# Kernel optimization log

Hardware: AMD Instinct MI355X
Metric: run time of the kernel (lower is better)

Reference implementation:

```python
import jax, jax.numpy as jnp
import numpy as np

N = 50000; E = 1600000; F = 128; H = 128; C = 40; G = 4
GRID = jnp.linspace(-2.0, 2.0, G)          # FastKAN default grid [-2, 2]
DENOM = 4.0 / (G - 1)                      # (grid_max - grid_min) / (num_grids - 1)
EPS = 1e-5
DIMS = [(F, H), (H, H), (F + 2 * H, C)]    # conv0, conv1, conv_out (skip concat)


def setup_inputs() -> dict:
    key = jax.random.key(0)
    ks = iter(jax.random.split(key, 64))
    inp = {}
    inp["x"] = jax.random.normal(next(ks), (N, F), jnp.float32)
    inp["edge_index"] = jax.random.randint(next(ks), (2, E), 0, N)
    for i, (di, do) in enumerate(DIMS):
        inp[f"c{i}_ln_g"] = jnp.ones((di,), jnp.float32)
        inp[f"c{i}_ln_b"] = jnp.zeros((di,), jnp.float32)
        inp[f"c{i}_sw"] = jax.random.normal(next(ks), (do, di * G), jnp.float32) * 0.1
        inp[f"c{i}_sb"] = jnp.zeros((do,), jnp.float32)
        inp[f"c{i}_bw"] = jax.random.normal(next(ks), (do, di), jnp.float32) * (1.0 / np.sqrt(di))
        inp[f"c{i}_bb"] = jnp.zeros((do,), jnp.float32)
        inp[f"c{i}_bias"] = jnp.zeros((do,), jnp.float32)   # GCNConv output bias
    inp["bn_g"] = jnp.ones((H,), jnp.float32)
    inp["bn_b"] = jnp.zeros((H,), jnp.float32)
    return inp


def _fkan(h, lg, lb, sw, sb, bw, bb):
    # FastKANLayer: LayerNorm -> RBF basis -> spline linear, plus SiLU base branch
    mu = h.mean(-1, keepdims=True)
    var = jnp.mean(jnp.square(h - mu), -1, keepdims=True)
    hn = (h - mu) * jax.lax.rsqrt(var + EPS) * lg + lb
    basis = jnp.exp(-jnp.square((hn[..., None] - GRID) / DENOM))  # [N, d, G]
    basis = basis.reshape(h.shape[0], -1)                          # [N, d*G]
    return basis @ sw.T + sb + jax.nn.silu(h) @ bw.T + bb


def _forward(x, edge_index, params, bn_g, bn_b):
    # gcn_norm with self-loops, symmetric normalization
    row = jnp.concatenate([edge_index[0], jnp.arange(N)])
    col = jnp.concatenate([edge_index[1], jnp.arange(N)])
    deg = jax.ops.segment_sum(jnp.ones_like(row, jnp.float32), col, num_segments=N)
    dis = jnp.where(deg > 0, jax.lax.rsqrt(jnp.maximum(deg, 1e-12)), 0.0)
    norm = dis[row] * dis[col]

    def conv(h, p):
        hw = _fkan(h, *p[:6])  # lin = FKANLayer applied before propagate
        return jax.ops.segment_sum(norm[:, None] * hw[row], col, num_segments=N) + p[6]

    def bn(h):  # BatchNorm1d, training-mode batch stats (biased var); dropout p=0
        mu = h.mean(0)
        var = jnp.mean(jnp.square(h - mu), 0)
        return (h - mu) * jax.lax.rsqrt(var + EPS) * bn_g + bn_b

    skips = [x]
    h = x
    for p in params[:-1]:
        h = bn(conv(h, p))
        skips.append(h)
    h = jnp.concatenate(skips, axis=1)  # skip=True
    return conv(h, params[-1])


def reference(x, edge_index, c0_ln_g, c0_ln_b, c0_sw, c0_sb, c0_bw, c0_bb, c0_bias,
              c1_ln_g, c1_ln_b, c1_sw, c1_sb, c1_bw, c1_bb, c1_bias,
              c2_ln_g, c2_ln_b, c2_sw, c2_sb, c2_bw, c2_bb, c2_bias, bn_g, bn_b):
    params = [
        (c0_ln_g, c0_ln_b, c0_sw, c0_sb, c0_bw, c0_bb, c0_bias),
        (c1_ln_g, c1_ln_b, c1_sw, c1_sb, c1_bw, c1_bb, c1_bias),
        (c2_ln_g, c2_ln_b, c2_sw, c2_sb, c2_bw, c2_bb, c2_bias),
    ]
    return _forward(x, edge_index, params, bn_g, bn_b)
```

## Files before the change

### kernel.cpp

```cpp
#include <hip/hip_runtime.h>
#include <math.h>

constexpr int NN = 50000;
constexpr int NE = 1600000;
constexpr float LN_EPS = 1e-5f;

constexpr int NBKT  = 8;
constexpr int SPAN  = NN / NBKT;
constexpr int CHUNK = 8192;
constexpr int NB1   = (NE + CHUNK - 1) / CHUNK;
constexpr int NSB   = (NN + 255) / 256;

typedef __attribute__((ext_vector_type(8))) short short8;
typedef __attribute__((ext_vector_type(4))) float f32x4;

__device__ __forceinline__ short f2bf(float f)
{
    unsigned u = __builtin_bit_cast(unsigned, f);
    u += 0x7fffu + ((u >> 16) & 1u);
    return (short)(u >> 16);
}

__device__ __forceinline__ float2 bf2x2(unsigned p)
{
    float2 r;
    r.x = __builtin_bit_cast(float, p << 16);
    r.y = __builtin_bit_cast(float, p & 0xffff0000u);
    return r;
}

__global__ __launch_bounds__(256) void csr_hist(const int* __restrict__ col,
                                                int* __restrict__ degi,
                                                int* __restrict__ histo)
{
    __shared__ int hcnt[NBKT];
    const int tid = threadIdx.x;
    if (tid < NBKT) hcnt[tid] = 0;
    __syncthreads();
    const int e0 = blockIdx.x * CHUNK;
    const int e1 = min(e0 + CHUNK, NE);
    for (int e = e0 + tid; e < e1; e += 256) {
        int c = col[e];
        atomicAdd(&degi[c], 1);
        atomicAdd(&hcnt[(unsigned)c / (unsigned)SPAN], 1);
    }
    __syncthreads();
    if (tid < NBKT) histo[tid * NB1 + blockIdx.x] = hcnt[tid];
}

__global__ __launch_bounds__(256) void csr_scan2(int* __restrict__ histo)
{
    constexpr int M = NBKT * NB1;
    constexpr int T = (M + 255) / 256;
    __shared__ int part[256];
    const int t = threadIdx.x;
    int v[T];
    int s = 0;
    #pragma unroll
    for (int j = 0; j < T; ++j) {
        int i = t * T + j;
        v[j] = (i < M) ? histo[i] : 0;
        s += v[j];
    }
    part[t] = s;
    __syncthreads();
    for (int d = 1; d < 256; d <<= 1) {
        int add = (t >= d) ? part[t - d] : 0;
        __syncthreads();
        part[t] += add;
        __syncthreads();
    }
    int run = part[t] - s;
    #pragma unroll
    for (int j = 0; j < T; ++j) {
        int i = t * T + j;
        if (i < M) { histo[i] = run; run += v[j]; }
    }
}

__global__ __launch_bounds__(256) void csr_part(const int* __restrict__ ei,
                                                const int* __restrict__ histo,
                                                uint2* __restrict__ staging)
{
    __shared__ int lcur[NBKT];
    const int tid = threadIdx.x;
    if (tid < NBKT) lcur[tid] = histo[tid * NB1 + blockIdx.x];
    __syncthreads();
    const int e0 = blockIdx.x * CHUNK;
    const int e1 = min(e0 + CHUNK, NE);
    for (int e = e0 + tid; e < e1; e += 256) {
        int r = ei[e];
        int c = ei[NE + e];
        int slot = atomicAdd(&lcur[(unsigned)c / (unsigned)SPAN], 1);
        staging[slot] = make_uint2((unsigned)r, (unsigned)c);
    }
}

template<int PB2>
__global__ __launch_bounds__(256) void csr_scatter(const uint2* __restrict__ staging,
                                                   const int* __restrict__ off,
                                                   int* __restrict__ cur,
                                                   int* __restrict__ rows)
{
    const int b   = blockIdx.x & (NBKT - 1);
    const int blk = blockIdx.x >> 3;
    const int base = off[b * SPAN];
    const int end  = off[(b + 1) * SPAN];
    for (int i = base + blk * 256 + threadIdx.x; i < end; i += PB2 * 256) {
        uint2 e = staging[i];
        int p = off[e.y] + atomicAdd(&cur[e.y], 1);
        rows[p] = (int)e.x;
    }
}

__global__ void dis_kernel(const int* __restrict__ degi, float* __restrict__ dis)
{
    int i = blockIdx.x * 256 + threadIdx.x;
    if (i < NN) dis[i] = rsqrtf((float)degi[i] + 1.0f);
}

__global__ __launch_bounds__(256) void scan_p1(const int* __restrict__ deg,
                                               int* __restrict__ off,
                                               int* __restrict__ partials)
{
    __shared__ int sh[256];
    const int t = threadIdx.x;
    const int i = blockIdx.x * 256 + t;
    int v = (i < NN) ? deg[i] : 0;
    sh[t] = v;
    __syncthreads();
    for (int d = 1; d < 256; d <<= 1) {
        int add = (t >= d) ? sh[t - d] : 0;
        __syncthreads();
        sh[t] += add;
        __syncthreads();
    }
    if (i < NN) off[i] = sh[t] - v;
    if (t == 255) partials[blockIdx.x] = sh[255];
}

__global__ __launch_bounds__(256) void scan_p2(int* __restrict__ partials)
{
    __shared__ int sh[256];
    const int t = threadIdx.x;
    int v = (t < NSB) ? partials[t] : 0;
    sh[t] = v;
    __syncthreads();
    for (int d = 1; d < 256; d <<= 1) {
        int add = (t >= d) ? sh[t - d] : 0;
        __syncthreads();
        sh[t] += add;
        __syncthreads();
    }
    if (t < NSB) partials[t] = sh[t] - v;
    if (t == 255) partials[NSB] = sh[255];
}

__global__ __launch_bounds__(256) void scan_p3(int* __restrict__ off,
                                               const int* __restrict__ partials)
{
    const int i = blockIdx.x * 256 + threadIdx.x;
    if (i < NN) off[i] += partials[blockIdx.x];
    if (i == 0) off[NN] = partials[NSB];
}

__global__ void pack_frag(const float* __restrict__ sw, const float* __restrict__ bw,
                          short* __restrict__ wtf, int D, int OT, int DO, int total)
{
    int idx = blockIdx.x * 256 + threadIdx.x;
    if (idx >= total) return;
    int j8   = idx & 7;
    int lane = (idx >> 3) & 63;
    int rest = idx >> 9;
    int ot = rest % OT, kk = rest / OT;
    int g4 = lane >> 4;
    int s  = kk * 8 + j8;
    int f  = g4 * (D / 4) + s / 5;
    int g5 = s % 5;
    int o  = ot * 16 + (lane & 15);
    float val = 0.f;
    if (o < DO) val = (g5 < 4) ? sw[o * D * 4 + f * 4 + g5] : bw[o * D + f];
    wtf[idx] = f2bf(val);
}

__global__ void bn_id(float2* __restrict__ bnp)
{
    bnp[threadIdx.x] = make_float2(1.0f, 0.0f);
}

__global__ void bn_final(const float* __restrict__ stats, const float* __restrict__ g,
                         const float* __restrict__ b, float2* __restrict__ dst)
{
    int c = threadIdx.x;
    float mu  = stats[c] * (1.0f / NN);
    float var = stats[c + 128] * (1.0f / NN) - mu * mu;
    float rs  = rsqrtf(var + LN_EPS);
    float sc  = rs * g[c];
    dst[c] = make_float2(sc, b[c] - mu * sc);
}

template<int DO, int OT, int KKC, bool BN>
__global__ __launch_bounds__(256, 4) void fkan_rd(
    const float* __restrict__ s0, const float2* __restrict__ bnp,
    const float* __restrict__ ln_g, const float* __restrict__ ln_b,
    const short* __restrict__ wtf, const float* __restrict__ sb, const float* __restrict__ bb,
    short* __restrict__ out)
{
    const int tid  = threadIdx.x;
    const int wv   = tid >> 6, lane = tid & 63;
    const int m    = lane & 15, q = lane >> 4;
    const int gnode = blockIdx.x * 64 + wv * 16 + m;
    const int snode = (gnode < NN) ? gnode : (NN - 1);

    float4 v[8];
    float sum = 0.f, sq = 0.f;
    #pragma unroll
    for (int i = 0; i < 8; ++i) {
        int f = q * 32 + i * 4;
        float4 t = *(const float4*)&s0[snode * 128 + f];
        if constexpr (BN) {
            float4 ba = *(const float4*)&bnp[f];
            float4 bc = *(const float4*)&bnp[f + 2];
            t.x = fmaf(t.x, ba.x, ba.y);
            t.y = fmaf(t.y, ba.z, ba.w);
            t.z = fmaf(t.z, bc.x, bc.y);
            t.w = fmaf(t.w, bc.z, bc.w);
        }
        v[i] = t;
        sum += (t.x + t.y) + (t.z + t.w);
        sq  += (t.x * t.x + t.y * t.y) + (t.z * t.z + t.w * t.w);
    }
    sum += __shfl_xor(sum, 16); sum += __shfl_xor(sum, 32);
    sq  += __shfl_xor(sq, 16);  sq  += __shfl_xor(sq, 32);
    const float mu   = sum * (1.0f / 128.0f);
    const float rstd = rsqrtf(sq * (1.0f / 128.0f) - mu * mu + LN_EPS);

    f32x4 acc[OT];
    #pragma unroll
    for (int ot = 0; ot < OT; ++ot) acc[ot] = f32x4{0.f, 0.f, 0.f, 0.f};

    union AU { unsigned u[4]; short8 s; };

    #pragma unroll
    for (int pl = 0; pl < KKC / 5; ++pl) {
        float hn[8], slv[8];
        {
            float4 lg0 = *(const float4*)&ln_g[q * 32 + pl * 8];
            float4 lg1 = *(const float4*)&ln_g[q * 32 + pl * 8 + 4];
            float4 lb0 = *(const float4*)&ln_b[q * 32 + pl * 8];
            float4 lb1 = *(const float4*)&ln_b[q * 32 + pl * 8 + 4];
            float4 va = v[pl * 2], vb = v[pl * 2 + 1];
            hn[0] = (va.x - mu) * rstd * lg0.x + lb0.x;
            hn[1] = (va.y - mu) * rstd * lg0.y + lb0.y;
            hn[2] = (va.z - mu) * rstd * lg0.z + lb0.z;
            hn[3] = (va.w - mu) * rstd * lg0.w + lb0.w;
            hn[4] = (vb.x - mu) * rstd * lg1.x + lb1.x;
            hn[5] = (vb.y - mu) * rstd * lg1.y + lb1.y;
            hn[6] = (vb.z - mu) * rstd * lg1.z + lb1.z;
            hn[7] = (vb.w - mu) * rstd * lg1.w + lb1.w;
            slv[0] = va.x / (1.0f + __expf(-va.x));
            slv[1] = va.y / (1.0f + __expf(-va.y));
            slv[2] = va.z / (1.0f + __expf(-va.z));
            slv[3] = va.w / (1.0f + __expf(-va.w));
            slv[4] = vb.x / (1.0f + __expf(-vb.x));
            slv[5] = vb.y / (1.0f + __expf(-vb.y));
            slv[6] = vb.z / (1.0f + __expf(-vb.z));
            slv[7] = vb.w / (1.0f + __expf(-vb.w));
        }
        const short* bp = wtf + (pl * 5) * OT * 512 + lane * 8;
        #pragma unroll
        for (int c = 0; c < 5; ++c) {
            AU a;
            #pragma unroll
            for (int i = 0; i < 4; ++i) {
                unsigned v2[2];
                #pragma unroll
                for (int h = 0; h < 2; ++h) {
                    int s  = c * 8 + 2 * i + h;
                    int fl = s / 5;
                    int g  = s % 5;
                    if (g == 4) {
                        v2[h] = (unsigned)(unsigned short)f2bf(slv[fl]);
                    } else {
                        float t = hn[fl] * 0.75f + (1.5f - (float)g);
                        float e = __expf(-t * t);
                        v2[h] = (unsigned)(unsigned short)f2bf(e);
                    }
                }
                a.u[i] = (v2[0] & 0xffffu) | (v2[1] << 16);
            }
            #pragma unroll
            for (int ot = 0; ot < OT; ++ot) {
                short8 b = *(const short8*)(bp + (c * OT + ot) * 512);
                acc[ot] = __builtin_amdgcn_mfma_f32_16x16x32_bf16(a.s, b, acc[ot], 0, 0, 0);
            }
        }
    }

    const int nrow0 = blockIdx.x * 64 + wv * 16 + q * 4;
    #pragma unroll
    for (int ot = 0; ot < OT; ++ot) {
        int o = ot * 16 + m;
        if (o < DO) {
            float cb = sb[o] + bb[o];
            #pragma unroll
            for (int r = 0; r < 4; ++r) {
                int nr = nrow0 + r;
                if (nr < NN) out[nr * DO + o] = f2bf(acc[ot][r] + cb);
            }
        }
    }
}

template<int D, int DO, int OT, int KKC, int NODES, int WPE, bool RAWLDS, bool BN>
__global__ __launch_bounds__(NODES * 4, WPE) void fkan_reg(
    const float* __restrict__ s0, const float* __restrict__ s1, const float* __restrict__ s2,
    const float2* __restrict__ bnp,
    const float* __restrict__ ln_g, const float* __restrict__ ln_b,
    const short* __restrict__ wtf, const float* __restrict__ sb, const float* __restrict__ bb,
    short* __restrict__ out)
{
    constexpr int BW   = D / 4;
    constexpr int GBS  = BW + 1;
    constexpr int RS   = 4 * GBS + 1;
    constexpr int PPC  = KKC / 5;
    constexpr int NV   = RAWLDS ? 1 : (BW / 4);
    __shared__ unsigned pkL[NODES * RS];

    const int tid = threadIdx.x;
    const int anode = tid >> 2, q = tid & 3;
    const int gnode = blockIdx.x * NODES + anode;
    const int snode = (gnode < NN) ? gnode : (NN - 1);
    unsigned* prow = &pkL[anode * RS + q * GBS];

    float mu, rstd;
    float4 va[NV];
    {
        float sum = 0.f, sq = 0.f;
        #pragma unroll
        for (int i4 = 0; i4 < BW / 4; ++i4) {
            int f = q * BW + i4 * 4;
            const float* src = (D == 128) ? s0 : ((f < 128) ? s0 : (f < 256) ? s1 : s2);
            float4 v = *(const float4*)&src[snode * 128 + (f & 127)];
            if constexpr (BN) {
                float4 ba = *(const float4*)&bnp[f];
                float4 bc = *(const float4*)&bnp[f + 2];
                v.x = fmaf(v.x, ba.x, ba.y);
                v.y = fmaf(v.y, ba.z, ba.w);
                v.z = fmaf(v.z, bc.x, bc.y);
                v.w = fmaf(v.w, bc.z, bc.w);
            }
            if constexpr (RAWLDS) {
                prow[i4 * 4 + 0] = __builtin_bit_cast(unsigned, v.x);
                prow[i4 * 4 + 1] = __builtin_bit_cast(unsigned, v.y);
                prow[i4 * 4 + 2] = __builtin_bit_cast(unsigned, v.z);
                prow[i4 * 4 + 3] = __builtin_bit_cast(unsigned, v.w);
            } else {
                va[i4] = v;
            }
            sum += (v.x + v.y) + (v.z + v.w);
            sq  += (v.x * v.x + v.y * v.y) + (v.z * v.z + v.w * v.w);
        }
        sum += __shfl_xor(sum, 1); sum += __shfl_xor(sum, 2);
        sq  += __shfl_xor(sq, 1);  sq  += __shfl_xor(sq, 2);
        mu   = sum * (1.0f / D);
        rstd = rsqrtf(sq * (1.0f / D) - mu * mu + LN_EPS);
    }

    #pragma unroll
    for (int i4 = 0; i4 < BW / 4; ++i4) {
        int f = q * BW + i4 * 4;
        float4 v;
        if constexpr (RAWLDS) {
            v.x = __builtin_bit_cast(float, prow[i4 * 4 + 0]);
            v.y = __builtin_bit_cast(float, prow[i4 * 4 + 1]);
            v.z = __builtin_bit_cast(float, prow[i4 * 4 + 2]);
            v.w = __builtin_bit_cast(float, prow[i4 * 4 + 3]);
        } else {
            v = va[i4];
        }
        float4 lg = *(const float4*)&ln_g[f];
        float4 lb = *(const float4*)&ln_b[f];
        float hn[4], sl[4];
        hn[0] = (v.x - mu) * rstd * lg.x + lb.x;
        hn[1] = (v.y - mu) * rstd * lg.y + lb.y;
        hn[2] = (v.z - mu) * rstd * lg.z + lb.z;
        hn[3] = (v.w - mu) * rstd * lg.w + lb.w;
        sl[0] = v.x / (1.0f + __expf(-v.x));
        sl[1] = v.y / (1.0f + __expf(-v.y));
        sl[2] = v.z / (1.0f + __expf(-v.z));
        sl[3] = v.w / (1.0f + __expf(-v.w));
        #pragma unroll
        for (int k = 0; k < 4; ++k)
            prow[i4 * 4 + k] = ((unsigned)(unsigned short)f2bf(hn[k]) << 16)
                             | ((unsigned)(unsigned short)f2bf(sl[k]) & 0xffffu);
    }
    __syncthreads();

    const int wv = tid >> 6, lane = tid & 63;
    const int m = lane & 15, g4 = lane >> 4;
    const unsigned* pkb = &pkL[(wv * 16 + m) * RS + g4 * GBS];

    f32x4 acc[OT];
    #pragma unroll
    for (int ot = 0; ot < OT; ++ot) acc[ot] = f32x4{0.f, 0.f, 0.f, 0.f};

    union AU { unsigned u[4]; short8 s; };

    for (int pl = 0; pl < PPC; ++pl) {
        const unsigned* pp = pkb + pl * 8;
        const short* bp = wtf + (pl * 5) * OT * 512 + lane * 8;
        #pragma unroll
        for (int c = 0; c < 5; ++c) {
            constexpr int FL0[5] = {0, 1, 3, 4, 6};
            constexpr int NF[5]  = {2, 3, 2, 3, 2};
            unsigned p[3];
            float h75[3];
            #pragma unroll
            for (int i = 0; i < 3; ++i) {
                if (i < NF[c]) {
                    p[i]   = pp[FL0[c] + i];
                    h75[i] = __builtin_bit_cast(float, p[i] & 0xffff0000u) * 0.75f;
                }
            }
            AU a;
            #pragma unroll
            for (int i = 0; i < 4; ++i) {
                unsigned v2[2];
                #pragma unroll
                for (int h = 0; h < 2; ++h) {
                    int sl = c * 8 + 2 * i + h;
                    int fl = sl / 5 - FL0[c];
                    int g  = sl % 5;
                    if (g == 4) {
                        v2[h] = p[fl] & 0xffffu;
                    } else {
                        float t = h75[fl] + (1.5f - (float)g);
                        float e = __expf(-t * t);
                        v2[h] = (unsigned)(unsigned short)f2bf(e);
                    }
                }
                a.u[i] = (v2[0] & 0xffffu) | (v2[1] << 16);
            }
            #pragma unroll
            for (int ot = 0; ot < OT; ++ot) {
                short8 b = *(const short8*)(bp + (c * OT + ot) * 512);
                acc[ot] = __builtin_amdgcn_mfma_f32_16x16x32_bf16(a.s, b, acc[ot], 0, 0, 0);
            }
        }
    }

    const int nrow0 = blockIdx.x * NODES + wv * 16 + g4 * 4;
    #pragma unroll
    for (int ot = 0; ot < OT; ++ot) {
        int o = ot * 16 + m;
        if (o < DO) {
            float cb = sb[o] + bb[o];
            #pragma unroll
            for (int r = 0; r < 4; ++r) {
                int nr = nrow0 + r;
                if (nr < NN) out[nr * DO + o] = f2bf(acc[ot][r] + cb);
            }
        }
    }
}

template<int DO>
__global__ __launch_bounds__(64) void agg_gather_bf16(
    const int* __restrict__ off, const int* __restrict__ rows,
    const float* __restrict__ dis, const short* __restrict__ hwb,
    const float* __restrict__ bias, float* __restrict__ out)
{
    constexpr int ACT = DO / 2;
    const int n   = blockIdx.x;
    const int tid = threadIdx.x;
    __shared__ int   srow[64];
    __shared__ float swgt[64];

    const int e0 = off[n], e1 = off[n + 1];
    const float dn = dis[n];
    float ax = 0.f, ay = 0.f;
    if (tid < ACT) {
        unsigned p = *(const unsigned*)&hwb[n * DO + 2 * tid];
        float2 v = bf2x2(p);
        ax = dn * dn * v.x + bias[2 * tid];
        ay = dn * dn * v.y + bias[2 * tid + 1];
    }

    for (int t0 = e0; t0 < e1; t0 += 64) {
        const int nt = min(64, e1 - t0);
        if (tid < nt) {
            int r = rows[t0 + tid];
            srow[tid] = r;
            swgt[tid] = dn * dis[r];
        }
        __syncthreads();
        if (tid < ACT) {
            #pragma unroll 4
            for (int j = 0; j < nt; ++j) {
                unsigned p = *(const unsigned*)&hwb[srow[j] * DO + 2 * tid];
                float2 v = bf2x2(p);
                float w = swgt[j];
                ax += w * v.x;
                ay += w * v.y;
            }
        }
        __syncthreads();
    }
    if (tid < ACT) {
        out[n * DO + 2 * tid]     = ax;
        out[n * DO + 2 * tid + 1] = ay;
    }
}

__global__ void bn_stats(const float* __restrict__ h, float* __restrict__ stats)
{
    __shared__ float s1[256], s2[256];
    int c = threadIdx.x & 127;
    int half = threadIdx.x >> 7;
    float sum = 0.f, sq = 0.f;
    for (int n = blockIdx.x * 2 + half; n < NN; n += 512) {
        float v = h[n * 128 + c];
        sum += v; sq += v * v;
    }
    s1[threadIdx.x] = sum; s2[threadIdx.x] = sq;
    __syncthreads();
    if (half == 0) {
        s1[c] += s1[c + 128]; s2[c] += s2[c + 128];
        atomicAdd(&stats[c],        s1[c]);
        atomicAdd(&stats[c + 128],  s2[c]);
    }
}

extern "C" void kernel_launch(void* const* d_in, const int* in_sizes, int n_in,
                              void* d_out, int out_size, void* d_ws, size_t ws_size,
                              hipStream_t stream)
{
    auto F = [&](int i) { return (const float*)d_in[i]; };
    const float* x  = F(0);
    const int*   ei = (const int*)d_in[1];
    const float* bn_g = F(23);
    const float* bn_b = F(24);

    short*  wtf0 = (short*)d_ws;
    short*  wtf1 = wtf0 + 81920;
    short*  wtf2 = wtf1 + 81920;
    short*  hwb  = wtf2 + 92160;
    float*  dis  = (float*)(hwb + 6400000);
    float2* bnp  = (float2*)(dis + 50000);
    float*  h1   = (float*)(bnp + 384);
    float*  h2   = h1 + 6400000;
    float*  stats = h2 + 6400000;
    int*    degi = (int*)(stats + 256);
    int*    off  = degi + 50000;
    int*    cur  = off + 50001;
    int*    rows = cur + 50000;
    int*    histo = rows + NE;
    int*    partials = histo + NBKT * NB1;
    uint2*  staging = (uint2*)h1;
    float*  outf = (float*)d_out;

    (void)hipMemsetAsync(degi, 0, 50000 * sizeof(int), stream);
    (void)hipMemsetAsync(cur,  0, 50000 * sizeof(int), stream);
    csr_hist<<<NB1, 256, 0, stream>>>(ei + NE, degi, histo);
    dis_kernel<<<(NN + 255) / 256, 256, 0, stream>>>(degi, dis);
    scan_p1<<<NSB, 256, 0, stream>>>(degi, off, partials);
    scan_p2<<<1, 256, 0, stream>>>(partials);
    scan_p3<<<NSB, 256, 0, stream>>>(off, partials);
    csr_scan2<<<1, 256, 0, stream>>>(histo);
    csr_part<<<NB1, 256, 0, stream>>>(ei, histo, staging);
    csr_scatter<128><<<128 * NBKT, 256, 0, stream>>>(staging, off, cur, rows);

    pack_frag<<<(81920 + 255) / 256, 256, 0, stream>>>(F(4),  F(6),  wtf0, 128, 8, 128, 81920);
    pack_frag<<<(81920 + 255) / 256, 256, 0, stream>>>(F(11), F(13), wtf1, 128, 8, 128, 81920);
    pack_frag<<<(92160 + 255) / 256, 256, 0, stream>>>(F(18), F(20), wtf2, 384, 3, 40,  92160);
    bn_id<<<1, 128, 0, stream>>>(bnp);

    const int gridN64 = (NN + 63) / 64;
    const int gridN16 = (NN + 15) / 16;

    fkan_rd<128, 8, 20, false><<<gridN64, 256, 0, stream>>>(x,
        nullptr, F(2), F(3), wtf0, F(5), F(7), hwb);
    agg_gather_bf16<128><<<NN, 64, 0, stream>>>(off, rows, dis, hwb, F(8), h1);
    (void)hipMemsetAsync(stats, 0, 256 * sizeof(float), stream);
    bn_stats<<<256, 256, 0, stream>>>(h1, stats);
    bn_final<<<1, 128, 0, stream>>>(stats, bn_g, bn_b, bnp + 128);

    fkan_rd<128, 8, 20, true><<<gridN64, 256, 0, stream>>>(h1,
        bnp + 128, F(9), F(10), wtf1, F(12), F(14), hwb);
    agg_gather_bf16<128><<<NN, 64, 0, stream>>>(off, rows, dis, hwb, F(15), h2);
    (void)hipMemsetAsync(stats, 0, 256 * sizeof(float), stream);
    bn_stats<<<256, 256, 0, stream>>>(h2, stats);
    bn_final<<<1, 128, 0, stream>>>(stats, bn_g, bn_b, bnp + 256);

    fkan_reg<384, 40, 3, 60, 16, 2, true, true><<<gridN16, 64, 0, stream>>>(x, h1, h2,
        bnp, F(16), F(17), wtf2, F(19), F(21), hwb);
    agg_gather_bf16<40><<<NN, 64, 0, stream>>>(off, rows, dis, hwb, F(22), outf);
}
```

Baseline: 540.1 us.

## Split final-layer LayerNorm stats into separate kernel and compute basis in registers

```diff
diff --git a/kernel.cpp b/kernel.cpp
--- a/kernel.cpp
+++ b/kernel.cpp
@@ -197,6 +197,40 @@
     float rs  = rsqrtf(var + LN_EPS);
     float sc  = rs * g[c];
     dst[c] = make_float2(sc, b[c] - mu * sc);
+}
+
+template<int D>
+__global__ __launch_bounds__(256) void ln_stats(
+    const float* __restrict__ s0, const float* __restrict__ s1, const float* __restrict__ s2,
+    const float2* __restrict__ bnp, float2* __restrict__ murstd)
+{
+    constexpr int BW = D / 4;
+    const int tid = threadIdx.x;
+    const int anode = tid >> 2, q = tid & 3;
+    const int gnode = blockIdx.x * 64 + anode;
+    const int snode = (gnode < NN) ? gnode : (NN - 1);
+    float sum = 0.f, sq = 0.f;
+    #pragma unroll
+    for (int i4 = 0; i4 < BW / 4; ++i4) {
+        int f = q * BW + i4 * 4;
+        const float* src = (f < 128) ? s0 : (f < 256) ? s1 : s2;
+        float4 v = *(const float4*)&src[snode * 128 + (f & 127)];
+        float4 ba = *(const float4*)&bnp[f];
+        float4 bc = *(const float4*)&bnp[f + 2];
+        v.x = fmaf(v.x, ba.x, ba.y);
+        v.y = fmaf(v.y, ba.z, ba.w);
+        v.z = fmaf(v.z, bc.x, bc.y);
+        v.w = fmaf(v.w, bc.z, bc.w);
+        sum += (v.x + v.y) + (v.z + v.w);
+        sq  += (v.x * v.x + v.y * v.y) + (v.z * v.z + v.w * v.w);
+    }
+    sum += __shfl_xor(sum, 1); sum += __shfl_xor(sum, 2);
+    sq  += __shfl_xor(sq, 1);  sq  += __shfl_xor(sq, 2);
+    if (q == 0 && gnode < NN) {
+        float mu   = sum * (1.0f / D);
+        float rstd = rsqrtf(sq * (1.0f / D) - mu * mu + LN_EPS);
+        murstd[gnode] = make_float2(mu, rstd);
+    }
 }
 
 template<int DO, int OT, int KKC, bool BN>
@@ -312,94 +346,21 @@
     }
 }
 
-template<int D, int DO, int OT, int KKC, int NODES, int WPE, bool RAWLDS, bool BN>
-__global__ __launch_bounds__(NODES * 4, WPE) void fkan_reg(
+template<int DO, int OT, int KKC>
+__global__ __launch_bounds__(256, 4) void fkan_rd2(
     const float* __restrict__ s0, const float* __restrict__ s1, const float* __restrict__ s2,
-    const float2* __restrict__ bnp,
+    const float2* __restrict__ bnp, const float2* __restrict__ murstd,
     const float* __restrict__ ln_g, const float* __restrict__ ln_b,
     const short* __restrict__ wtf, const float* __restrict__ sb, const float* __restrict__ bb,
     short* __restrict__ out)
 {
-    constexpr int BW   = D / 4;
-    constexpr int GBS  = BW + 1;
-    constexpr int RS   = 4 * GBS + 1;
-    constexpr int PPC  = KKC / 5;
-    constexpr int NV   = RAWLDS ? 1 : (BW / 4);
-    __shared__ unsigned pkL[NODES * RS];
-
-    const int tid = threadIdx.x;
-    const int anode = tid >> 2, q = tid & 3;
-    const int gnode = blockIdx.x * NODES + anode;
+    const int tid  = threadIdx.x;
+    const int wv   = tid >> 6, lane = tid & 63;
+    const int m    = lane & 15, q = lane >> 4;
+    const int gnode = blockIdx.x * 64 + wv * 16 + m;
     const int snode = (gnode < NN) ? gnode : (NN - 1);
-    unsigned* prow = &pkL[anode * RS + q * GBS];
-
-    float mu, rstd;
-    float4 va[NV];
-    {
-        float sum = 0.f, sq = 0.f;
-        #pragma unroll
-        for (int i4 = 0; i4 < BW / 4; ++i4) {
-            int f = q * BW + i4 * 4;
-            const float* src = (D == 128) ? s0 : ((f < 128) ? s0 : (f < 256) ? s1 : s2);
-            float4 v = *(const float4*)&src[snode * 128 + (f & 127)];
-            if constexpr (BN) {
-                float4 ba = *(const float4*)&bnp[f];
-                float4 bc = *(const float4*)&bnp[f + 2];
-                v.x = fmaf(v.x, ba.x, ba.y);
-                v.y = fmaf(v.y, ba.z, ba.w);
-                v.z = fmaf(v.z, bc.x, bc.y);
-                v.w = fmaf(v.w, bc.z, bc.w);
-            }
-            if constexpr (RAWLDS) {
-                prow[i4 * 4 + 0] = __builtin_bit_cast(unsigned, v.x);
-                prow[i4 * 4 + 1] = __builtin_bit_cast(unsigned, v.y);
-                prow[i4 * 4 + 2] = __builtin_bit_cast(unsigned, v.z);
-                prow[i4 * 4 + 3] = __builtin_bit_cast(unsigned, v.w);
-            } else {
-                va[i4] = v;
-            }
-            sum += (v.x + v.y) + (v.z + v.w);
-            sq  += (v.x * v.x + v.y * v.y) + (v.z * v.z + v.w * v.w);
-        }
-        sum += __shfl_xor(sum, 1); sum += __shfl_xor(sum, 2);
-        sq  += __shfl_xor(sq, 1);  sq  += __shfl_xor(sq, 2);
-        mu   = sum * (1.0f / D);
-        rstd = rsqrtf(sq * (1.0f / D) - mu * mu + LN_EPS);
-    }
-
-    #pragma unroll
-    for (int i4 = 0; i4 < BW / 4; ++i4) {
-        int f = q * BW + i4 * 4;
-        float4 v;
-        if constexpr (RAWLDS) {
-            v.x = __builtin_bit_cast(float, prow[i4 * 4 + 0]);
-            v.y = __builtin_bit_cast(float, prow[i4 * 4 + 1]);
-            v.z = __builtin_bit_cast(float, prow[i4 * 4 + 2]);
-            v.w = __builtin_bit_cast(float, prow[i4 * 4 + 3]);
-        } else {
-            v = va[i4];
-        }
-        float4 lg = *(const float4*)&ln_g[f];
-        float4 lb = *(const float4*)&ln_b[f];
-        float hn[4], sl[4];
-        hn[0] = (v.x - mu) * rstd * lg.x + lb.x;
-        hn[1] = (v.y - mu) * rstd * lg.y + lb.y;
-        hn[2] = (v.z - mu) * rstd * lg.z + lb.z;
-        hn[3] = (v.w - mu) * rstd * lg.w + lb.w;
-        sl[0] = v.x / (1.0f + __expf(-v.x));
-        sl[1] = v.y / (1.0f + __expf(-v.y));
-        sl[2] = v.z / (1.0f + __expf(-v.z));
-        sl[3] = v.w / (1.0f + __expf(-v.w));
-        #pragma unroll
-        for (int k = 0; k < 4; ++k)
-            prow[i4 * 4 + k] = ((unsigned)(unsigned short)f2bf(hn[k]) << 16)
-                             | ((unsigned)(unsigned short)f2bf(sl[k]) & 0xffffu);
-    }
-    __syncthreads();
-
-    const int wv = tid >> 6, lane = tid & 63;
-    const int m = lane & 15, g4 = lane >> 4;
-    const unsigned* pkb = &pkL[(wv * 16 + m) * RS + g4 * GBS];
+    const float2 ms = murstd[snode];
+    const float mu = ms.x, rstd = ms.y;
 
     f32x4 acc[OT];
     #pragma unroll
@@ -407,35 +368,68 @@
 
     union AU { unsigned u[4]; short8 s; };
 
-    for (int pl = 0; pl < PPC; ++pl) {
-        const unsigned* pp = pkb + pl * 8;
+    #pragma unroll
+    for (int pl = 0; pl < KKC / 5; ++pl) {
+        const int fa = q * 96 + pl * 8;
+        const int fb = fa + 4;
+        float4 va, vb;
+        {
+            const float* sa = (fa < 128) ? s0 : (fa < 256) ? s1 : s2;
+            const float* sc = (fb < 128) ? s0 : (fb < 256) ? s1 : s2;
+            va = *(const float4*)&sa[snode * 128 + (fa & 127)];
+            vb = *(const float4*)&sc[snode * 128 + (fb & 127)];
+            float4 b0 = *(const float4*)&bnp[fa];
+            float4 b1 = *(const float4*)&bnp[fa + 2];
+            float4 b2 = *(const float4*)&bnp[fb];
+            float4 b3 = *(const float4*)&bnp[fb + 2];
+            va.x = fmaf(va.x, b0.x, b0.y);
+            va.y = fmaf(va.y, b0.z, b0.w);
+            va.z = fmaf(va.z, b1.x, b1.y);
+            va.w = fmaf(va.w, b1.z, b1.w);
+            vb.x = fmaf(vb.x, b2.x, b2.y);
+            vb.y = fmaf(vb.y, b2.z, b2.w);
+            vb.z = fmaf(vb.z, b3.x, b3.y);
+            vb.w = fmaf(vb.w, b3.z, b3.w);
+        }
+        float hn[8], slv[8];
+        {
+            float4 lg0 = *(const float4*)&ln_g[fa];
+            float4 lg1 = *(const float4*)&ln_g[fb];
+            float4 lb0 = *(const float4*)&ln_b[fa];
+            float4 lb1 = *(const float4*)&ln_b[fb];
+            hn[0] = (va.x - mu) * rstd * lg0.x + lb0.x;
+            hn[1] = (va.y - mu) * rstd * lg0.y + lb0.y;
+            hn[2] = (va.z - mu) * rstd * lg0.z + lb0.z;
+            hn[3] = (va.w - mu) * rstd * lg0.w + lb0.w;
+            hn[4] = (vb.x - mu) * rstd * lg1.x + lb1.x;
+            hn[5] = (vb.y - mu) * rstd * lg1.y + lb1.y;
+            hn[6] = (vb.z - mu) * rstd * lg1.z + lb1.z;
+            hn[7] = (vb.w - mu) * rstd * lg1.w + lb1.w;
+            slv[0] = va.x / (1.0f + __expf(-va.x));
+            slv[1] = va.y / (1.0f + __expf(-va.y));
+            slv[2] = va.z / (1.0f + __expf(-va.z));
+            slv[3] = va.w / (1.0f + __expf(-va.w));
+            slv[4] = vb.x / (1.0f + __expf(-vb.x));
+            slv[5] = vb.y / (1.0f + __expf(-vb.y));
+            slv[6] = vb.z / (1.0f + __expf(-vb.z));
+            slv[7] = vb.w / (1.0f + __expf(-vb.w));
+        }
         const short* bp = wtf + (pl * 5) * OT * 512 + lane * 8;
         #pragma unroll
         for (int c = 0; c < 5; ++c) {
-            constexpr int FL0[5] = {0, 1, 3, 4, 6};
-            constexpr int NF[5]  = {2, 3, 2, 3, 2};
-            unsigned p[3];
-            float h75[3];
-            #pragma unroll
-            for (int i = 0; i < 3; ++i) {
-                if (i < NF[c]) {
-                    p[i]   = pp[FL0[c] + i];
-                    h75[i] = __builtin_bit_cast(float, p[i] & 0xffff0000u) * 0.75f;
-                }
-            }
             AU a;
             #pragma unroll
             for (int i = 0; i < 4; ++i) {
                 unsigned v2[2];
                 #pragma unroll
                 for (int h = 0; h < 2; ++h) {
-                    int sl = c * 8 + 2 * i + h;
-                    int fl = sl / 5 - FL0[c];
-                    int g  = sl % 5;
+                    int s  = c * 8 + 2 * i + h;
+                    int fl = s / 5;
+                    int g  = s % 5;
                     if (g == 4) {
-                        v2[h] = p[fl] & 0xffffu;
+                        v2[h] = (unsigned)(unsigned short)f2bf(slv[fl]);
                     } else {
-                        float t = h75[fl] + (1.5f - (float)g);
+                        float t = hn[fl] * 0.75f + (1.5f - (float)g);
                         float e = __expf(-t * t);
                         v2[h] = (unsigned)(unsigned short)f2bf(e);
                     }
@@ -450,7 +444,7 @@
         }
     }
 
-    const int nrow0 = blockIdx.x * NODES + wv * 16 + g4 * 4;
+    const int nrow0 = blockIdx.x * 64 + wv * 16 + q * 4;
     #pragma unroll
     for (int ot = 0; ot < OT; ++ot) {
         int o = ot * 16 + m;
@@ -548,7 +542,8 @@
     short*  hwb  = wtf2 + 92160;
     float*  dis  = (float*)(hwb + 6400000);
     float2* bnp  = (float2*)(dis + 50000);
-    float*  h1   = (float*)(bnp + 384);
+    float2* murstd = bnp + 384;
+    float*  h1   = (float*)(murstd + 50000);
     float*  h2   = h1 + 6400000;
     float*  stats = h2 + 6400000;
     int*    degi = (int*)(stats + 256);
@@ -577,7 +572,6 @@
     bn_id<<<1, 128, 0, stream>>>(bnp);
 
     const int gridN64 = (NN + 63) / 64;
-    const int gridN16 = (NN + 15) / 16;
 
     fkan_rd<128, 8, 20, false><<<gridN64, 256, 0, stream>>>(x,
         nullptr, F(2), F(3), wtf0, F(5), F(7), hwb);
@@ -593,7 +587,8 @@
     bn_stats<<<256, 256, 0, stream>>>(h2, stats);
     bn_final<<<1, 128, 0, stream>>>(stats, bn_g, bn_b, bnp + 256);
 
-    fkan_reg<384, 40, 3, 60, 16, 2, true, true><<<gridN16, 64, 0, stream>>>(x, h1, h2,
-        bnp, F(16), F(17), wtf2, F(19), F(21), hwb);
+    ln_stats<384><<<gridN64, 256, 0, stream>>>(x, h1, h2, bnp, murstd);
+    fkan_rd2<40, 3, 60><<<gridN64, 256, 0, stream>>>(x, h1, h2,
+        bnp, murstd, F(16), F(17), wtf2, F(19), F(21), hwb);
     agg_gather_bf16<40><<<NN, 64, 0, stream>>>(off, rows, dis, hwb, F(22), outf);
 }
```

Result: slower. 560.3 us (+3.7%).
